# Kernel tuning notes

Measured on AMD Instinct MI355X. Metric: run time of the kernel, lower is better.

The kernel has to match this reference:

```python
import jax, jax.numpy as jnp
import numpy as np

N, E, D_IN, H, D = 170000, 1200000, 128, 4, 32
NEG_SLOPE = 0.2


def setup_inputs() -> dict:
    key = jax.random.key(0)
    ks = jax.random.split(key, 8)
    x = jax.random.normal(ks[0], (N, D_IN), dtype=jnp.float32)
    # xavier-normal-ish scale for linear weights
    W_embed = jax.random.normal(ks[1], (D_IN, H * D), dtype=jnp.float32) * (2.0 / (D_IN + H * D)) ** 0.5
    a_src = jax.random.normal(ks[2], (H, D), dtype=jnp.float32) * (2.0 / (1 + H * D)) ** 0.5
    a_dst = jax.random.normal(ks[3], (H, D), dtype=jnp.float32) * (2.0 / (1 + H * D)) ** 0.5
    W_lin = jax.random.normal(ks[4], (D_IN, H * D), dtype=jnp.float32) * (2.0 / (D_IN + H * D)) ** 0.5
    bias = jnp.zeros((H * D,), dtype=jnp.float32)
    src = jax.random.randint(ks[5], (E,), 0, N, dtype=jnp.int32)
    dst = jax.random.randint(ks[6], (E,), 0, N, dtype=jnp.int32)
    return {"x": x, "W_embed": W_embed, "a_src": a_src, "a_dst": a_dst,
            "W_lin": W_lin, "bias": bias, "src": src, "dst": dst}


def reference(x, W_embed, a_src, a_dst, W_lin, bias, src, dst):
    n = x.shape[0]
    # node projections: [N, H, D]
    h = (x @ W_embed).reshape(n, H, D)
    dot_src = jnp.einsum('nhd,hd->nh', h, a_src)  # [N, H]
    dot_dst = jnp.einsum('nhd,hd->nh', h, a_dst)  # [N, H]
    # edge attention logits: leaky_relu(dot_src[u] + dot_dst[v])  [E, H]
    z = dot_src[src] + dot_dst[dst]
    logit = jnp.where(z >= 0, z, NEG_SLOPE * z)
    # edge softmax over incoming edges of each destination node
    m = jax.ops.segment_max(logit, dst, num_segments=n)          # [N, H]
    e = jnp.exp(logit - m[dst])                                   # [E, H]
    denom = jax.ops.segment_sum(e, dst, num_segments=n)          # [N, H]
    prob = e / denom[dst]                                         # [E, H]
    # weighted scatter-sum aggregation: sum_e prob_e * h[src_e]
    msg = h[src] * prob[:, :, None]                               # [E, H, D]
    out = jax.ops.segment_sum(msg, dst, num_segments=n)          # [N, H, D]
    out = out.reshape(n, H * D)
    out = out + x @ W_lin
    out = out + bias[None, :]
    return out
```

## Files before the change

### kernel.cpp

```cpp
#include <hip/hip_runtime.h>
#include <hip/hip_bf16.h>

static constexpr int   N_NODES   = 170000;
static constexpr int   E_EDGES   = 1200000;
static constexpr float NEG_SLOPE = 0.2f;

typedef __attribute__((ext_vector_type(8))) short bfrag8;
typedef __attribute__((ext_vector_type(4))) float facc4;

__device__ __forceinline__ short f2bf(float f) {
    __hip_bfloat16 h = __float2bfloat16(f);
    return *reinterpret_cast<short*>(&h);
}

__global__ void wt_convert_kernel(const float* __restrict__ We,
                                  const float* __restrict__ Wl,
                                  short* __restrict__ WtG)
{
    const int k = blockIdx.x;
    const int t = threadIdx.x;
    if (t < 128) WtG[t * 128 + k] = f2bf(We[k * 128 + t]);
    else         WtG[t * 128 + k] = f2bf(Wl[k * 128 + (t - 128)]);
}

__global__ void init_kernel(int* __restrict__ deg) {
    int i = blockIdx.x * blockDim.x + threadIdx.x;
    if (i < N_NODES) deg[i] = 0;
}

__global__ void hist_kernel(const int* __restrict__ dst, int* __restrict__ deg) {
    int e = blockIdx.x * blockDim.x + threadIdx.x;
    if (e < E_EDGES) atomicAdd(&deg[dst[e]], 1);
}

__global__ __launch_bounds__(256) void scan_local_kernel(
    const int* __restrict__ deg, int* __restrict__ row_ptr, int* __restrict__ bsum)
{
    __shared__ int sh[256];
    const int t = threadIdx.x;
    const int base = blockIdx.x * 1024 + t * 4;
    int v0 = (base + 0 < N_NODES) ? deg[base + 0] : 0;
    int v1 = (base + 1 < N_NODES) ? deg[base + 1] : 0;
    int v2 = (base + 2 < N_NODES) ? deg[base + 2] : 0;
    int v3 = (base + 3 < N_NODES) ? deg[base + 3] : 0;
    const int tot = v0 + v1 + v2 + v3;
    sh[t] = tot;
    __syncthreads();
    for (int off = 1; off < 256; off <<= 1) {
        int add = (t >= off) ? sh[t - off] : 0;
        __syncthreads();
        sh[t] += add;
        __syncthreads();
    }
    const int excl = sh[t] - tot;
    if (base + 0 < N_NODES) row_ptr[base + 0] = excl;
    if (base + 1 < N_NODES) row_ptr[base + 1] = excl + v0;
    if (base + 2 < N_NODES) row_ptr[base + 2] = excl + v0 + v1;
    if (base + 3 < N_NODES) row_ptr[base + 3] = excl + v0 + v1 + v2;
    if (t == 255) bsum[blockIdx.x] = sh[255];
}

__global__ __launch_bounds__(256) void scan_block_kernel(
    const int* __restrict__ bsum, int* __restrict__ boff, int nblk)
{
    __shared__ int sh[256];
    const int t = threadIdx.x;
    const int v = (t < nblk) ? bsum[t] : 0;
    sh[t] = v;
    __syncthreads();
    for (int off = 1; off < 256; off <<= 1) {
        int add = (t >= off) ? sh[t - off] : 0;
        __syncthreads();
        sh[t] += add;
        __syncthreads();
    }
    boff[t] = sh[t] - v;
}

__global__ void scan_add_kernel(int* __restrict__ row_ptr,
                                const int* __restrict__ boff,
                                int* __restrict__ fill)
{
    int i = blockIdx.x * blockDim.x + threadIdx.x;
    if (i < N_NODES) {
        int v = row_ptr[i] + boff[i >> 10];
        row_ptr[i] = v;
        fill[i] = v;
    }
    if (i == 0) row_ptr[N_NODES] = E_EDGES;
}

static constexpr int LDA = 136;

__global__ __launch_bounds__(256) void mfma_gemm_kernel(
    const float* __restrict__ x,
    const short* __restrict__ WtG,
    const float* __restrict__ bias,
    const float* __restrict__ a_srcp,
    const float* __restrict__ a_dstp,
    short* __restrict__ hbuf,
    float* __restrict__ dsrc,
    float* __restrict__ ddst,
    float* __restrict__ outp)
{
    __shared__ short As[64 * LDA];
    __shared__ short Bs[128 * LDA];
    const int tid  = threadIdx.x;
    const int half = blockIdx.y;
    const long row0 = (long)blockIdx.x * 64;

    #pragma unroll
    for (int it = 0; it < 8; ++it) {
        const int idx = it * 256 + tid;
        const int n   = idx >> 4;
        const int kc  = (idx & 15) * 8;
        *(int4*)&Bs[n * LDA + kc] =
            *(const int4*)&WtG[(half * 128 + n) * 128 + kc];
    }
    #pragma unroll
    for (int it = 0; it < 8; ++it) {
        const int idx = it * 256 + tid;
        const int r = idx >> 5;
        const int j = idx & 31;
        const long row = row0 + r;
        float4 v = make_float4(0.f, 0.f, 0.f, 0.f);
        if (row < N_NODES) v = ((const float4*)x)[row * 32 + j];
        uint u0 = (uint)(unsigned short)f2bf(v.x) | ((uint)(unsigned short)f2bf(v.y) << 16);
        uint u1 = (uint)(unsigned short)f2bf(v.z) | ((uint)(unsigned short)f2bf(v.w) << 16);
        *(uint2*)&As[r * LDA + j * 4] = make_uint2(u0, u1);
    }
    __syncthreads();

    const int w    = tid >> 6;
    const int l    = tid & 63;
    const int col  = l & 15;
    const int quad = l >> 4;
    const int mrow = w * 16 + col;

    facc4 acc[8];
    #pragma unroll
    for (int t = 0; t < 8; ++t) acc[t] = (facc4)(0.f);

    #pragma unroll
    for (int ks = 0; ks < 4; ++ks) {
        const bfrag8 a = *(const bfrag8*)&As[mrow * LDA + ks * 32 + quad * 8];
        #pragma unroll
        for (int t = 0; t < 8; ++t) {
            const bfrag8 b = *(const bfrag8*)&Bs[(t * 16 + col) * LDA + ks * 32 + quad * 8];
            acc[t] = __builtin_amdgcn_mfma_f32_16x16x32_bf16(a, b, acc[t], 0, 0, 0);
        }
    }

    const long rbase = row0 + w * 16 + quad * 4;
    if (half == 0) {
        float as[8], ad[8];
        #pragma unroll
        for (int t = 0; t < 8; ++t) {
            as[t] = a_srcp[t * 16 + col];
            ad[t] = a_dstp[t * 16 + col];
        }
        #pragma unroll
        for (int r = 0; r < 4; ++r) {
            const long m = rbase + r;
            if (m >= N_NODES) continue;
            float ps[4] = {0.f, 0.f, 0.f, 0.f};
            float pd[4] = {0.f, 0.f, 0.f, 0.f};
            #pragma unroll
            for (int t = 0; t < 8; ++t) {
                hbuf[m * 128 + t * 16 + col] = f2bf(acc[t][r]);
                ps[t >> 1] += acc[t][r] * as[t];
                pd[t >> 1] += acc[t][r] * ad[t];
            }
            #pragma unroll
            for (int mask = 1; mask < 16; mask <<= 1) {
                #pragma unroll
                for (int hh = 0; hh < 4; ++hh) {
                    ps[hh] += __shfl_xor(ps[hh], mask, 16);
                    pd[hh] += __shfl_xor(pd[hh], mask, 16);
                }
            }
            if (col == 0) {
                ((float4*)dsrc)[m] = make_float4(ps[0], ps[1], ps[2], ps[3]);
                ((float4*)ddst)[m] = make_float4(pd[0], pd[1], pd[2], pd[3]);
            }
        }
    } else {
        #pragma unroll
        for (int t = 0; t < 8; ++t) {
            const float bv = bias[t * 16 + col];
            #pragma unroll
            for (int r = 0; r < 4; ++r) {
                const long m = rbase + r;
                if (m < N_NODES) outp[m * 128 + t * 16 + col] = acc[t][r] + bv;
            }
        }
    }
}

__global__ void csr_place_kernel(const int* __restrict__ src,
                                 const int* __restrict__ dst,
                                 int* __restrict__ fill,
                                 int* __restrict__ srcs)
{
    int e = blockIdx.x * blockDim.x + threadIdx.x;
    if (e >= E_EDGES) return;
    const int p = atomicAdd(&fill[dst[e]], 1);
    srcs[p] = src[e];
}

__global__ __launch_bounds__(256) void agg_kernel(
    const int* __restrict__ row_ptr, const int* __restrict__ srcs,
    const float* __restrict__ dsrc, const float* __restrict__ ddst,
    const short* __restrict__ hbuf, float* __restrict__ outp)
{
    const long node = (long)blockIdx.x * 4 + (threadIdx.x >> 6);
    if (node >= N_NODES) return;
    const int lane = threadIdx.x & 63;
    const int head = lane >> 4;
    const int start = __builtin_amdgcn_readfirstlane(row_ptr[node]);
    const int end   = __builtin_amdgcn_readfirstlane(row_ptr[node + 1]);
    if (start == end) return;

    const float dd = ddst[node * 4 + head];

    float a0 = 0.f, a1 = 0.f, dn = 0.f;
    for (int j = start; j < end; ++j) {
        const int s = __builtin_amdgcn_readfirstlane(srcs[j]);
        float z = dsrc[s * 4 + head] + dd;
        z = (z >= 0.f) ? z : NEG_SLOPE * z;
        const float wgt = __expf(z);
        dn += wgt;
        const uint hv = *(const uint*)&hbuf[(long)s * 128 + (lane << 1)];
        a0 += wgt * __uint_as_float(hv << 16);
        a1 += wgt * __uint_as_float(hv & 0xFFFF0000u);
    }
    const float inv = 1.f / dn;
    float2* op = (float2*)&outp[node * 128 + (lane << 1)];
    float2 o = *op;
    o.x += a0 * inv;
    o.y += a1 * inv;
    *op = o;
}

extern "C" void kernel_launch(void* const* d_in, const int* in_sizes, int n_in,
                              void* d_out, int out_size, void* d_ws, size_t ws_size,
                              hipStream_t stream)
{
    const float* x       = (const float*)d_in[0];
    const float* W_embed = (const float*)d_in[1];
    const float* a_src   = (const float*)d_in[2];
    const float* a_dst   = (const float*)d_in[3];
    const float* W_lin   = (const float*)d_in[4];
    const float* bias    = (const float*)d_in[5];
    const int*   src     = (const int*)d_in[6];
    const int*   dst     = (const int*)d_in[7];
    float* outp = (float*)d_out;

    char* ws = (char*)d_ws;
    short* WtG   = (short*)ws;  ws += (size_t)256 * 128 * sizeof(short);
    short* hbuf  = (short*)ws;  ws += (size_t)N_NODES * 128 * sizeof(short);
    int*   srcs  = (int*)ws;    ws += (size_t)E_EDGES * sizeof(int);
    float* dsrc  = (float*)ws;  ws += (size_t)N_NODES * 4 * sizeof(float);
    float* ddst  = (float*)ws;  ws += (size_t)N_NODES * 4 * sizeof(float);
    int*   deg   = (int*)ws;    ws += (size_t)N_NODES * sizeof(int);
    int*   fill  = (int*)ws;    ws += (size_t)N_NODES * sizeof(int);
    int*   rowp  = (int*)ws;    ws += (size_t)(N_NODES + 16) * sizeof(int);
    int*   bsum  = (int*)ws;    ws += 256 * sizeof(int);
    int*   boff  = (int*)ws;    ws += 256 * sizeof(int);

    const int SCAN_BLKS = (N_NODES + 1023) / 1024;

    wt_convert_kernel<<<128, 256, 0, stream>>>(W_embed, W_lin, WtG);
    init_kernel<<<(N_NODES + 255) / 256, 256, 0, stream>>>(deg);
    hist_kernel<<<(E_EDGES + 255) / 256, 256, 0, stream>>>(dst, deg);
    scan_local_kernel<<<SCAN_BLKS, 256, 0, stream>>>(deg, rowp, bsum);
    scan_block_kernel<<<1, 256, 0, stream>>>(bsum, boff, SCAN_BLKS);
    scan_add_kernel<<<(N_NODES + 255) / 256, 256, 0, stream>>>(rowp, boff, fill);

    dim3 ggrid((N_NODES + 63) / 64, 2);
    mfma_gemm_kernel<<<ggrid, 256, 0, stream>>>(
        x, WtG, bias, a_src, a_dst, hbuf, dsrc, ddst, outp);

    csr_place_kernel<<<(E_EDGES + 255) / 256, 256, 0, stream>>>(src, dst, fill, srcs);

    agg_kernel<<<(N_NODES + 3) / 4, 256, 0, stream>>>(
        rowp, srcs, dsrc, ddst, hbuf, outp);
}
```

Baseline: 455.3 us.

## Reuse x tile across both GEMM halves and batch edge weights in aggregation

After: 466.6 us. 2.5% more time.

```diff
diff --git a/kernel.cpp b/kernel.cpp
--- a/kernel.cpp
+++ b/kernel.cpp
@@ -21,11 +21,6 @@
     const int t = threadIdx.x;
     if (t < 128) WtG[t * 128 + k] = f2bf(We[k * 128 + t]);
     else         WtG[t * 128 + k] = f2bf(Wl[k * 128 + (t - 128)]);
-}
-
-__global__ void init_kernel(int* __restrict__ deg) {
-    int i = blockIdx.x * blockDim.x + threadIdx.x;
-    if (i < N_NODES) deg[i] = 0;
 }
 
 __global__ void hist_kernel(const int* __restrict__ dst, int* __restrict__ deg) {
@@ -106,17 +101,8 @@
     __shared__ short As[64 * LDA];
     __shared__ short Bs[128 * LDA];
     const int tid  = threadIdx.x;
-    const int half = blockIdx.y;
     const long row0 = (long)blockIdx.x * 64;
 
-    #pragma unroll
-    for (int it = 0; it < 8; ++it) {
-        const int idx = it * 256 + tid;
-        const int n   = idx >> 4;
-        const int kc  = (idx & 15) * 8;
-        *(int4*)&Bs[n * LDA + kc] =
-            *(const int4*)&WtG[(half * 128 + n) * 128 + kc];
-    }
     #pragma unroll
     for (int it = 0; it < 8; ++it) {
         const int idx = it * 256 + tid;
@@ -129,69 +115,81 @@
         uint u1 = (uint)(unsigned short)f2bf(v.z) | ((uint)(unsigned short)f2bf(v.w) << 16);
         *(uint2*)&As[r * LDA + j * 4] = make_uint2(u0, u1);
     }
-    __syncthreads();
 
     const int w    = tid >> 6;
     const int l    = tid & 63;
     const int col  = l & 15;
     const int quad = l >> 4;
     const int mrow = w * 16 + col;
-
-    facc4 acc[8];
-    #pragma unroll
-    for (int t = 0; t < 8; ++t) acc[t] = (facc4)(0.f);
-
-    #pragma unroll
-    for (int ks = 0; ks < 4; ++ks) {
-        const bfrag8 a = *(const bfrag8*)&As[mrow * LDA + ks * 32 + quad * 8];
+    const long rbase = row0 + w * 16 + quad * 4;
+
+    for (int half = 0; half < 2; ++half) {
         #pragma unroll
-        for (int t = 0; t < 8; ++t) {
-            const bfrag8 b = *(const bfrag8*)&Bs[(t * 16 + col) * LDA + ks * 32 + quad * 8];
-            acc[t] = __builtin_amdgcn_mfma_f32_16x16x32_bf16(a, b, acc[t], 0, 0, 0);
-        }
-    }
-
-    const long rbase = row0 + w * 16 + quad * 4;
-    if (half == 0) {
-        float as[8], ad[8];
+        for (int it = 0; it < 8; ++it) {
+            const int idx = it * 256 + tid;
+            const int n   = idx >> 4;
+            const int kc  = (idx & 15) * 8;
+            *(int4*)&Bs[n * LDA + kc] =
+                *(const int4*)&WtG[(half * 128 + n) * 128 + kc];
+        }
+        __syncthreads();
+
+        facc4 acc[8];
         #pragma unroll
-        for (int t = 0; t < 8; ++t) {
-            as[t] = a_srcp[t * 16 + col];
-            ad[t] = a_dstp[t * 16 + col];
-        }
+        for (int t = 0; t < 8; ++t) acc[t] = (facc4)(0.f);
+
         #pragma unroll
-        for (int r = 0; r < 4; ++r) {
-            const long m = rbase + r;
-            if (m >= N_NODES) continue;
-            float ps[4] = {0.f, 0.f, 0.f, 0.f};
-            float pd[4] = {0.f, 0.f, 0.f, 0.f};
+        for (int ks = 0; ks < 4; ++ks) {
+            const bfrag8 a = *(const bfrag8*)&As[mrow * LDA + ks * 32 + quad * 8];
             #pragma unroll
             for (int t = 0; t < 8; ++t) {
-                hbuf[m * 128 + t * 16 + col] = f2bf(acc[t][r]);
-                ps[t >> 1] += acc[t][r] * as[t];
-                pd[t >> 1] += acc[t][r] * ad[t];
-            }
-            #pragma unroll
-            for (int mask = 1; mask < 16; mask <<= 1) {
-                #pragma unroll
-                for (int hh = 0; hh < 4; ++hh) {
-                    ps[hh] += __shfl_xor(ps[hh], mask, 16);
-                    pd[hh] += __shfl_xor(pd[hh], mask, 16);
-                }
-            }
-            if (col == 0) {
-                ((float4*)dsrc)[m] = make_float4(ps[0], ps[1], ps[2], ps[3]);
-                ((float4*)ddst)[m] = make_float4(pd[0], pd[1], pd[2], pd[3]);
-            }
-        }
-    } else {
-        #pragma unroll
-        for (int t = 0; t < 8; ++t) {
-            const float bv = bias[t * 16 + col];
+                const bfrag8 b = *(const bfrag8*)&Bs[(t * 16 + col) * LDA + ks * 32 + quad * 8];
+                acc[t] = __builtin_amdgcn_mfma_f32_16x16x32_bf16(a, b, acc[t], 0, 0, 0);
+            }
+        }
+        __syncthreads();
+
+        if (half == 0) {
+            float as[8], ad[8];
+            #pragma unroll
+            for (int t = 0; t < 8; ++t) {
+                as[t] = a_srcp[t * 16 + col];
+                ad[t] = a_dstp[t * 16 + col];
+            }
             #pragma unroll
             for (int r = 0; r < 4; ++r) {
                 const long m = rbase + r;
-                if (m < N_NODES) outp[m * 128 + t * 16 + col] = acc[t][r] + bv;
+                if (m >= N_NODES) continue;
+                float ps[4] = {0.f, 0.f, 0.f, 0.f};
+                float pd[4] = {0.f, 0.f, 0.f, 0.f};
+                #pragma unroll
+                for (int t = 0; t < 8; ++t) {
+                    hbuf[m * 128 + t * 16 + col] = f2bf(acc[t][r]);
+                    ps[t >> 1] += acc[t][r] * as[t];
+                    pd[t >> 1] += acc[t][r] * ad[t];
+                }
+                #pragma unroll
+                for (int mask = 1; mask < 16; mask <<= 1) {
+                    #pragma unroll
+                    for (int hh = 0; hh < 4; ++hh) {
+                        ps[hh] += __shfl_xor(ps[hh], mask, 16);
+                        pd[hh] += __shfl_xor(pd[hh], mask, 16);
+                    }
+                }
+                if (col == 0) {
+                    ((float4*)dsrc)[m] = make_float4(ps[0], ps[1], ps[2], ps[3]);
+                    ((float4*)ddst)[m] = make_float4(pd[0], pd[1], pd[2], pd[3]);
+                }
+            }
+        } else {
+            #pragma unroll
+            for (int t = 0; t < 8; ++t) {
+                const float bv = bias[t * 16 + col];
+                #pragma unroll
+                for (int r = 0; r < 4; ++r) {
+                    const long m = rbase + r;
+                    if (m < N_NODES) outp[m * 128 + t * 16 + col] = acc[t][r] + bv;
+                }
             }
         }
     }
@@ -213,29 +211,36 @@
     const float* __restrict__ dsrc, const float* __restrict__ ddst,
     const short* __restrict__ hbuf, float* __restrict__ outp)
 {
-    const long node = (long)blockIdx.x * 4 + (threadIdx.x >> 6);
+    const int node = blockIdx.x * 4 + (threadIdx.x >> 6);
     if (node >= N_NODES) return;
     const int lane = threadIdx.x & 63;
     const int head = lane >> 4;
-    const int start = __builtin_amdgcn_readfirstlane(row_ptr[node]);
-    const int end   = __builtin_amdgcn_readfirstlane(row_ptr[node + 1]);
+    const int start = row_ptr[node];
+    const int end   = row_ptr[node + 1];
     if (start == end) return;
 
-    const float dd = ddst[node * 4 + head];
+    const float ddp = ddst[node * 4 + (lane & 3)];
+    const int j0 = lane >> 2;
 
     float a0 = 0.f, a1 = 0.f, dn = 0.f;
-    for (int j = start; j < end; ++j) {
-        const int s = __builtin_amdgcn_readfirstlane(srcs[j]);
-        float z = dsrc[s * 4 + head] + dd;
+    for (int base = start; base < end; base += 16) {
+        const int degc = min(16, end - base);
+        const int sA = srcs[base + min(j0, degc - 1)];
+        float z = dsrc[sA * 4 + (lane & 3)] + ddp;
         z = (z >= 0.f) ? z : NEG_SLOPE * z;
-        const float wgt = __expf(z);
-        dn += wgt;
-        const uint hv = *(const uint*)&hbuf[(long)s * 128 + (lane << 1)];
-        a0 += wgt * __uint_as_float(hv << 16);
-        a1 += wgt * __uint_as_float(hv & 0xFFFF0000u);
+        const float wv = __expf(z);
+        #pragma unroll 4
+        for (int j = 0; j < degc; ++j) {
+            const int s    = __shfl(sA, 4 * j);
+            const float wgt = __shfl(wv, 4 * j + head);
+            dn += wgt;
+            const uint hv = *(const uint*)&hbuf[(size_t)s * 128 + (lane << 1)];
+            a0 += wgt * __uint_as_float(hv << 16);
+            a1 += wgt * __uint_as_float(hv & 0xFFFF0000u);
+        }
     }
     const float inv = 1.f / dn;
-    float2* op = (float2*)&outp[node * 128 + (lane << 1)];
+    float2* op = (float2*)&outp[(size_t)node * 128 + (lane << 1)];
     float2 o = *op;
     o.x += a0 * inv;
     o.y += a1 * inv;
@@ -271,14 +276,13 @@
     const int SCAN_BLKS = (N_NODES + 1023) / 1024;
 
     wt_convert_kernel<<<128, 256, 0, stream>>>(W_embed, W_lin, WtG);
-    init_kernel<<<(N_NODES + 255) / 256, 256, 0, stream>>>(deg);
+    hipMemsetAsync(deg, 0, (size_t)N_NODES * sizeof(int), stream);
     hist_kernel<<<(E_EDGES + 255) / 256, 256, 0, stream>>>(dst, deg);
     scan_local_kernel<<<SCAN_BLKS, 256, 0, stream>>>(deg, rowp, bsum);
     scan_block_kernel<<<1, 256, 0, stream>>>(bsum, boff, SCAN_BLKS);
     scan_add_kernel<<<(N_NODES + 255) / 256, 256, 0, stream>>>(rowp, boff, fill);
 
-    dim3 ggrid((N_NODES + 63) / 64, 2);
-    mfma_gemm_kernel<<<ggrid, 256, 0, stream>>>(
+    mfma_gemm_kernel<<<(N_NODES + 63) / 64, 256, 0, stream>>>(
         x, WtG, bias, a_src, a_dst, hbuf, dsrc, ddst, outp);
 
     csr_place_kernel<<<(E_EDGES + 255) / 256, 256, 0, stream>>>(src, dst, fill, srcs);
```

## Fuse preprocessing kernels, merge GEMM halves with CSR placement, store linear term in bf16

Applied to the files above, without the earlier changes.

Result: slower. 464.8 us (+2.1%).

```diff
diff --git a/kernel.cpp b/kernel.cpp
--- a/kernel.cpp
+++ b/kernel.cpp
@@ -13,24 +13,21 @@
     return *reinterpret_cast<short*>(&h);
 }
 
-__global__ void wt_convert_kernel(const float* __restrict__ We,
-                                  const float* __restrict__ Wl,
-                                  short* __restrict__ WtG)
-{
-    const int k = blockIdx.x;
+__global__ void wt_hist_kernel(const float* __restrict__ We,
+                               const float* __restrict__ Wl,
+                               short* __restrict__ WtG,
+                               const int* __restrict__ dst,
+                               int* __restrict__ deg)
+{
     const int t = threadIdx.x;
-    if (t < 128) WtG[t * 128 + k] = f2bf(We[k * 128 + t]);
-    else         WtG[t * 128 + k] = f2bf(Wl[k * 128 + (t - 128)]);
-}
-
-__global__ void init_kernel(int* __restrict__ deg) {
-    int i = blockIdx.x * blockDim.x + threadIdx.x;
-    if (i < N_NODES) deg[i] = 0;
-}
-
-__global__ void hist_kernel(const int* __restrict__ dst, int* __restrict__ deg) {
-    int e = blockIdx.x * blockDim.x + threadIdx.x;
-    if (e < E_EDGES) atomicAdd(&deg[dst[e]], 1);
+    if (blockIdx.x < 128) {
+        const int k = blockIdx.x;
+        if (t < 128) WtG[t * 128 + k] = f2bf(We[k * 128 + t]);
+        else         WtG[t * 128 + k] = f2bf(Wl[k * 128 + (t - 128)]);
+    } else {
+        const int e = (blockIdx.x - 128) * 256 + t;
+        if (e < E_EDGES) atomicAdd(&deg[dst[e]], 1);
+    }
 }
 
 __global__ __launch_bounds__(256) void scan_local_kernel(
@@ -60,30 +57,18 @@
     if (t == 255) bsum[blockIdx.x] = sh[255];
 }
 
-__global__ __launch_bounds__(256) void scan_block_kernel(
-    const int* __restrict__ bsum, int* __restrict__ boff, int nblk)
-{
-    __shared__ int sh[256];
-    const int t = threadIdx.x;
-    const int v = (t < nblk) ? bsum[t] : 0;
-    sh[t] = v;
-    __syncthreads();
-    for (int off = 1; off < 256; off <<= 1) {
-        int add = (t >= off) ? sh[t - off] : 0;
-        __syncthreads();
-        sh[t] += add;
-        __syncthreads();
-    }
-    boff[t] = sh[t] - v;
-}
-
-__global__ void scan_add_kernel(int* __restrict__ row_ptr,
-                                const int* __restrict__ boff,
-                                int* __restrict__ fill)
-{
-    int i = blockIdx.x * blockDim.x + threadIdx.x;
+__global__ __launch_bounds__(256) void scan_finish_kernel(
+    const int* __restrict__ bsum, int* __restrict__ row_ptr, int* __restrict__ fill)
+{
+    const int i = blockIdx.x * 256 + threadIdx.x;
+    const int c = blockIdx.x >> 2;
+    const int lane = threadIdx.x & 63;
+    int partial = 0;
+    for (int j = lane; j < c; j += 64) partial += bsum[j];
+    #pragma unroll
+    for (int m = 1; m < 64; m <<= 1) partial += __shfl_xor(partial, m, 64);
     if (i < N_NODES) {
-        int v = row_ptr[i] + boff[i >> 10];
+        const int v = row_ptr[i] + partial;
         row_ptr[i] = v;
         fill[i] = v;
     }
@@ -91,32 +76,27 @@
 }
 
 static constexpr int LDA = 136;
-
-__global__ __launch_bounds__(256) void mfma_gemm_kernel(
+static constexpr int GEMM_BLOCKS = (N_NODES + 63) / 64;
+static constexpr int GEMM_THREADS = GEMM_BLOCKS * 256;
+
+__global__ __launch_bounds__(256) void gemm_csr_kernel(
     const float* __restrict__ x,
     const short* __restrict__ WtG,
     const float* __restrict__ bias,
     const float* __restrict__ a_srcp,
     const float* __restrict__ a_dstp,
     short* __restrict__ hbuf,
+    short* __restrict__ linbuf,
     float* __restrict__ dsrc,
     float* __restrict__ ddst,
-    float* __restrict__ outp)
+    const int* __restrict__ src, const int* __restrict__ dst,
+    int* __restrict__ fill, int* __restrict__ srcs)
 {
     __shared__ short As[64 * LDA];
     __shared__ short Bs[128 * LDA];
     const int tid  = threadIdx.x;
-    const int half = blockIdx.y;
     const long row0 = (long)blockIdx.x * 64;
 
-    #pragma unroll
-    for (int it = 0; it < 8; ++it) {
-        const int idx = it * 256 + tid;
-        const int n   = idx >> 4;
-        const int kc  = (idx & 15) * 8;
-        *(int4*)&Bs[n * LDA + kc] =
-            *(const int4*)&WtG[(half * 128 + n) * 128 + kc];
-    }
     #pragma unroll
     for (int it = 0; it < 8; ++it) {
         const int idx = it * 256 + tid;
@@ -129,117 +109,128 @@
         uint u1 = (uint)(unsigned short)f2bf(v.z) | ((uint)(unsigned short)f2bf(v.w) << 16);
         *(uint2*)&As[r * LDA + j * 4] = make_uint2(u0, u1);
     }
-    __syncthreads();
 
     const int w    = tid >> 6;
     const int l    = tid & 63;
     const int col  = l & 15;
     const int quad = l >> 4;
     const int mrow = w * 16 + col;
-
-    facc4 acc[8];
-    #pragma unroll
-    for (int t = 0; t < 8; ++t) acc[t] = (facc4)(0.f);
-
-    #pragma unroll
-    for (int ks = 0; ks < 4; ++ks) {
-        const bfrag8 a = *(const bfrag8*)&As[mrow * LDA + ks * 32 + quad * 8];
+    const long rbase = row0 + w * 16 + quad * 4;
+
+    for (int half = 0; half < 2; ++half) {
         #pragma unroll
-        for (int t = 0; t < 8; ++t) {
-            const bfrag8 b = *(const bfrag8*)&Bs[(t * 16 + col) * LDA + ks * 32 + quad * 8];
-            acc[t] = __builtin_amdgcn_mfma_f32_16x16x32_bf16(a, b, acc[t], 0, 0, 0);
-        }
-    }
-
-    const long rbase = row0 + w * 16 + quad * 4;
-    if (half == 0) {
-        float as[8], ad[8];
+        for (int it = 0; it < 8; ++it) {
+            const int idx = it * 256 + tid;
+            const int n   = idx >> 4;
+            const int kc  = (idx & 15) * 8;
+            *(int4*)&Bs[n * LDA + kc] =
+                *(const int4*)&WtG[(half * 128 + n) * 128 + kc];
+        }
+        __syncthreads();
+
+        facc4 acc[8];
         #pragma unroll
-        for (int t = 0; t < 8; ++t) {
-            as[t] = a_srcp[t * 16 + col];
-            ad[t] = a_dstp[t * 16 + col];
-        }
+        for (int t = 0; t < 8; ++t) acc[t] = (facc4)(0.f);
+
         #pragma unroll
-        for (int r = 0; r < 4; ++r) {
-            const long m = rbase + r;
-            if (m >= N_NODES) continue;
-            float ps[4] = {0.f, 0.f, 0.f, 0.f};
-            float pd[4] = {0.f, 0.f, 0.f, 0.f};
+        for (int ks = 0; ks < 4; ++ks) {
+            const bfrag8 a = *(const bfrag8*)&As[mrow * LDA + ks * 32 + quad * 8];
             #pragma unroll
             for (int t = 0; t < 8; ++t) {
-                hbuf[m * 128 + t * 16 + col] = f2bf(acc[t][r]);
-                ps[t >> 1] += acc[t][r] * as[t];
-                pd[t >> 1] += acc[t][r] * ad[t];
-            }
-            #pragma unroll
-            for (int mask = 1; mask < 16; mask <<= 1) {
-                #pragma unroll
-                for (int hh = 0; hh < 4; ++hh) {
-                    ps[hh] += __shfl_xor(ps[hh], mask, 16);
-                    pd[hh] += __shfl_xor(pd[hh], mask, 16);
-                }
-            }
-            if (col == 0) {
-                ((float4*)dsrc)[m] = make_float4(ps[0], ps[1], ps[2], ps[3]);
-                ((float4*)ddst)[m] = make_float4(pd[0], pd[1], pd[2], pd[3]);
-            }
-        }
-    } else {
-        #pragma unroll
-        for (int t = 0; t < 8; ++t) {
-            const float bv = bias[t * 16 + col];
+                const bfrag8 b = *(const bfrag8*)&Bs[(t * 16 + col) * LDA + ks * 32 + quad * 8];
+                acc[t] = __builtin_amdgcn_mfma_f32_16x16x32_bf16(a, b, acc[t], 0, 0, 0);
+            }
+        }
+        __syncthreads();
+
+        if (half == 0) {
+            float as[8], ad[8];
+            #pragma unroll
+            for (int t = 0; t < 8; ++t) {
+                as[t] = a_srcp[t * 16 + col];
+                ad[t] = a_dstp[t * 16 + col];
+            }
             #pragma unroll
             for (int r = 0; r < 4; ++r) {
                 const long m = rbase + r;
-                if (m < N_NODES) outp[m * 128 + t * 16 + col] = acc[t][r] + bv;
-            }
-        }
-    }
-}
-
-__global__ void csr_place_kernel(const int* __restrict__ src,
-                                 const int* __restrict__ dst,
-                                 int* __restrict__ fill,
-                                 int* __restrict__ srcs)
-{
-    int e = blockIdx.x * blockDim.x + threadIdx.x;
-    if (e >= E_EDGES) return;
-    const int p = atomicAdd(&fill[dst[e]], 1);
-    srcs[p] = src[e];
+                if (m >= N_NODES) continue;
+                float ps[4] = {0.f, 0.f, 0.f, 0.f};
+                float pd[4] = {0.f, 0.f, 0.f, 0.f};
+                #pragma unroll
+                for (int t = 0; t < 8; ++t) {
+                    hbuf[m * 128 + t * 16 + col] = f2bf(acc[t][r]);
+                    ps[t >> 1] += acc[t][r] * as[t];
+                    pd[t >> 1] += acc[t][r] * ad[t];
+                }
+                #pragma unroll
+                for (int mask = 1; mask < 16; mask <<= 1) {
+                    #pragma unroll
+                    for (int hh = 0; hh < 4; ++hh) {
+                        ps[hh] += __shfl_xor(ps[hh], mask, 16);
+                        pd[hh] += __shfl_xor(pd[hh], mask, 16);
+                    }
+                }
+                if (col == 0) {
+                    ((float4*)dsrc)[m] = make_float4(ps[0], ps[1], ps[2], ps[3]);
+                    ((float4*)ddst)[m] = make_float4(pd[0], pd[1], pd[2], pd[3]);
+                }
+            }
+        } else {
+            #pragma unroll
+            for (int t = 0; t < 8; ++t) {
+                const float bv = bias[t * 16 + col];
+                #pragma unroll
+                for (int r = 0; r < 4; ++r) {
+                    const long m = rbase + r;
+                    if (m < N_NODES) linbuf[m * 128 + t * 16 + col] = f2bf(acc[t][r] + bv);
+                }
+            }
+        }
+    }
+
+    const int gid = blockIdx.x * 256 + tid;
+    for (int e = gid; e < E_EDGES; e += GEMM_THREADS) {
+        const int p = atomicAdd(&fill[dst[e]], 1);
+        srcs[p] = src[e];
+    }
 }
 
 __global__ __launch_bounds__(256) void agg_kernel(
     const int* __restrict__ row_ptr, const int* __restrict__ srcs,
     const float* __restrict__ dsrc, const float* __restrict__ ddst,
-    const short* __restrict__ hbuf, float* __restrict__ outp)
-{
-    const long node = (long)blockIdx.x * 4 + (threadIdx.x >> 6);
+    const short* __restrict__ hbuf, const short* __restrict__ linbuf,
+    float* __restrict__ outp)
+{
+    const int node = blockIdx.x * 4 + (threadIdx.x >> 6);
     if (node >= N_NODES) return;
     const int lane = threadIdx.x & 63;
     const int head = lane >> 4;
-    const int start = __builtin_amdgcn_readfirstlane(row_ptr[node]);
-    const int end   = __builtin_amdgcn_readfirstlane(row_ptr[node + 1]);
-    if (start == end) return;
-
-    const float dd = ddst[node * 4 + head];
-
-    float a0 = 0.f, a1 = 0.f, dn = 0.f;
-    for (int j = start; j < end; ++j) {
-        const int s = __builtin_amdgcn_readfirstlane(srcs[j]);
-        float z = dsrc[s * 4 + head] + dd;
-        z = (z >= 0.f) ? z : NEG_SLOPE * z;
-        const float wgt = __expf(z);
-        dn += wgt;
-        const uint hv = *(const uint*)&hbuf[(long)s * 128 + (lane << 1)];
-        a0 += wgt * __uint_as_float(hv << 16);
-        a1 += wgt * __uint_as_float(hv & 0xFFFF0000u);
-    }
-    const float inv = 1.f / dn;
-    float2* op = (float2*)&outp[node * 128 + (lane << 1)];
-    float2 o = *op;
-    o.x += a0 * inv;
-    o.y += a1 * inv;
-    *op = o;
+    const int start = row_ptr[node];
+    const int end   = row_ptr[node + 1];
+
+    const uint lv = *(const uint*)&linbuf[(size_t)node * 128 + (lane << 1)];
+    float2 o;
+    o.x = __uint_as_float(lv << 16);
+    o.y = __uint_as_float(lv & 0xFFFF0000u);
+
+    if (start != end) {
+        const float dd = ddst[node * 4 + head];
+        float a0 = 0.f, a1 = 0.f, dn = 0.f;
+        for (int j = start; j < end; ++j) {
+            const int s = __builtin_amdgcn_readfirstlane(srcs[j]);
+            float z = dsrc[s * 4 + head] + dd;
+            z = (z >= 0.f) ? z : NEG_SLOPE * z;
+            const float wgt = __expf(z);
+            dn += wgt;
+            const uint hv = *(const uint*)&hbuf[(size_t)s * 128 + (lane << 1)];
+            a0 += wgt * __uint_as_float(hv << 16);
+            a1 += wgt * __uint_as_float(hv & 0xFFFF0000u);
+        }
+        const float inv = 1.f / dn;
+        o.x += a0 * inv;
+        o.y += a1 * inv;
+    }
+    *(float2*)&outp[(size_t)node * 128 + (lane << 1)] = o;
 }
 
 extern "C" void kernel_launch(void* const* d_in, const int* in_sizes, int n_in,
@@ -257,32 +248,32 @@
     float* outp = (float*)d_out;
 
     char* ws = (char*)d_ws;
-    short* WtG   = (short*)ws;  ws += (size_t)256 * 128 * sizeof(short);
-    short* hbuf  = (short*)ws;  ws += (size_t)N_NODES * 128 * sizeof(short);
-    int*   srcs  = (int*)ws;    ws += (size_t)E_EDGES * sizeof(int);
-    float* dsrc  = (float*)ws;  ws += (size_t)N_NODES * 4 * sizeof(float);
-    float* ddst  = (float*)ws;  ws += (size_t)N_NODES * 4 * sizeof(float);
-    int*   deg   = (int*)ws;    ws += (size_t)N_NODES * sizeof(int);
-    int*   fill  = (int*)ws;    ws += (size_t)N_NODES * sizeof(int);
-    int*   rowp  = (int*)ws;    ws += (size_t)(N_NODES + 16) * sizeof(int);
-    int*   bsum  = (int*)ws;    ws += 256 * sizeof(int);
-    int*   boff  = (int*)ws;    ws += 256 * sizeof(int);
+    short* WtG    = (short*)ws; ws += (size_t)256 * 128 * sizeof(short);
+    short* hbuf   = (short*)ws; ws += (size_t)N_NODES * 128 * sizeof(short);
+    short* linbuf = (short*)ws; ws += (size_t)N_NODES * 128 * sizeof(short);
+    int*   srcs   = (int*)ws;   ws += (size_t)E_EDGES * sizeof(int);
+    float* dsrc   = (float*)ws; ws += (size_t)N_NODES * 4 * sizeof(float);
+    float* ddst   = (float*)ws; ws += (size_t)N_NODES * 4 * sizeof(float);
+    int*   deg    = (int*)ws;   ws += (size_t)N_NODES * sizeof(int);
+    int*   fill   = (int*)ws;   ws += (size_t)N_NODES * sizeof(int);
+    int*   rowp   = (int*)ws;   ws += (size_t)(N_NODES + 16) * sizeof(int);
+    int*   bsum   = (int*)ws;   ws += 256 * sizeof(int);
 
     const int SCAN_BLKS = (N_NODES + 1023) / 1024;
 
-    wt_convert_kernel<<<128, 256, 0, stream>>>(W_embed, W_lin, WtG);
-    init_kernel<<<(N_NODES + 255) / 256, 256, 0, stream>>>(deg);
-    hist_kernel<<<(E_EDGES + 255) / 256, 256, 0, stream>>>(dst, deg);
+    hipMemsetAsync(deg, 0, (size_t)N_NODES * sizeof(int), stream);
+
+    wt_hist_kernel<<<128 + (E_EDGES + 255) / 256, 256, 0, stream>>>(
+        W_embed, W_lin, WtG, dst, deg);
+
     scan_local_kernel<<<SCAN_BLKS, 256, 0, stream>>>(deg, rowp, bsum);
-    scan_block_kernel<<<1, 256, 0, stream>>>(bsum, boff, SCAN_BLKS);
-    scan_add_kernel<<<(N_NODES + 255) / 256, 256, 0, stream>>>(rowp, boff, fill);
-
-    dim3 ggrid((N_NODES + 63) / 64, 2);
-    mfma_gemm_kernel<<<ggrid, 256, 0, stream>>>(
-        x, WtG, bias, a_src, a_dst, hbuf, dsrc, ddst, outp);
-
-    csr_place_kernel<<<(E_EDGES + 255) / 256, 256, 0, stream>>>(src, dst, fill, srcs);
+
+    scan_finish_kernel<<<(N_NODES + 255) / 256, 256, 0, stream>>>(bsum, rowp, fill);
+
+    gemm_csr_kernel<<<GEMM_BLOCKS, 256, 0, stream>>>(
+        x, WtG, bias, a_src, a_dst, hbuf, linbuf, dsrc, ddst,
+        src, dst, fill, srcs);
 
     agg_kernel<<<(N_NODES + 3) / 4, 256, 0, stream>>>(
-        rowp, srcs, dsrc, ddst, hbuf, outp);
-}
+        rowp, srcs, dsrc, ddst, hbuf, linbuf, outp);
+}
```
